# Kernel tuning notes

Measured on AMD Instinct MI355X. Metric: run time of the kernel, lower is better.

The kernel has to match this reference:

```python
import jax, jax.numpy as jnp
import numpy as np

V, D, NL, NC = 16, 256, 4, 2
MAXL, NSTATE, DCONV, EXPAND, HEADDIM = 1024, 64, 4, 2, 64
DIN = EXPAND * D            # 512 inner channels
H = DIN // HEADDIM          # 8 heads
P = HEADDIM                 # 64 head dim
CONV_DIM = DIN + 2 * NSTATE # 640 channels through depthwise conv
D_IN_PROJ = 2 * DIN + 2 * NSTATE + H  # 1160
B_, L_ = 2, 1024
EPS = 1e-5


def setup_inputs() -> dict:
    key = jax.random.key(0)
    ks = iter(jax.random.split(key, 32))

    def rn(shape, s=0.02):
        return jax.random.normal(next(ks), shape, jnp.float32) * s

    emb = rn((V, D)).at[4].set(0.0)  # padding_idx=4 row zeroed
    pos_emb = rn((MAXL, D))
    in_proj_w = rn((NL, D_IN_PROJ, D))
    conv_w = rn((NL, CONV_DIM, DCONV), 0.1)
    conv_b = rn((NL, CONV_DIM), 0.1)
    dt_bias = rn((NL, H), 0.5)
    A_log = jnp.log(jax.random.uniform(next(ks), (NL, H), jnp.float32, 1.0, 16.0))
    D_param = jnp.ones((NL, H), jnp.float32)
    norm_w = jnp.ones((NL, DIN), jnp.float32)
    out_proj_w = rn((NL, D, DIN))
    pooler_w = rn((D, D), 0.05)
    pooler_b = jnp.zeros((D,), jnp.float32)
    cls1_w = rn((D // 2, D), 0.05)
    cls1_b = jnp.zeros((D // 2,), jnp.float32)
    cls2_w = rn((NC, D // 2), 0.05)
    cls2_b = jnp.zeros((NC,), jnp.float32)
    input_ids = jax.random.randint(next(ks), (B_, L_), 0, V)
    return dict(input_ids=input_ids, emb=emb, pos_emb=pos_emb,
                in_proj_w=in_proj_w, conv_w=conv_w, conv_b=conv_b,
                dt_bias=dt_bias, A_log=A_log, D_param=D_param, norm_w=norm_w,
                out_proj_w=out_proj_w, pooler_w=pooler_w, pooler_b=pooler_b,
                cls1_w=cls1_w, cls1_b=cls1_b, cls2_w=cls2_w, cls2_b=cls2_b)


def _mamba2(x, Win, cw, cb, dtb, A_log, Dp, nw, Wout):
    Bsz, L, _ = x.shape
    zxbcdt = jnp.einsum('bld,pd->blp', x, Win)              # (B,L,2*DIN+2N+H)
    z = zxbcdt[..., :DIN]
    xBC = zxbcdt[..., DIN:DIN + CONV_DIM]
    dt = jax.nn.softplus(zxbcdt[..., -H:] + dtb)            # (B,L,H)
    # causal depthwise conv over time
    xBC = jnp.transpose(xBC, (0, 2, 1))                     # (B,C,L)
    xBC = jax.lax.conv_general_dilated(
        xBC, cw[:, None, :], (1,), [(DCONV - 1, 0)],
        dimension_numbers=('NCH', 'OIH', 'NCH'),
        feature_group_count=CONV_DIM)
    xBC = jax.nn.silu(jnp.transpose(xBC, (0, 2, 1)) + cb)   # (B,L,C)
    xs = xBC[..., :DIN].reshape(Bsz, L, H, P)
    Bm = xBC[..., DIN:DIN + NSTATE]                         # (B,L,N)
    Cm = xBC[..., DIN + NSTATE:]                            # (B,L,N)
    A = -jnp.exp(A_log)                                     # (H,)
    dA = jnp.exp(dt * A)                                    # (B,L,H)
    dBx = dt[..., None, None] * xs[..., None] * Bm[:, :, None, None, :]  # (B,L,H,P,N)

    def step(h, inp):
        dA_t, dBx_t, C_t = inp
        h = dA_t[:, :, None, None] * h + dBx_t              # (B,H,P,N)
        y = jnp.einsum('bhpn,bn->bhp', h, C_t)
        return h, y

    h0 = jnp.zeros((Bsz, H, P, NSTATE), x.dtype)
    _, y = jax.lax.scan(step, h0, (jnp.moveaxis(dA, 1, 0),
                                   jnp.moveaxis(dBx, 1, 0),
                                   jnp.moveaxis(Cm, 1, 0)))
    y = jnp.moveaxis(y, 0, 1) + Dp[None, None, :, None] * xs  # (B,L,H,P)
    y = y.reshape(Bsz, L, DIN) * jax.nn.silu(z)               # gated
    y = y * jax.lax.rsqrt(jnp.mean(y * y, axis=-1, keepdims=True) + EPS) * nw
    return jnp.einsum('bld,od->blo', y, Wout)


def reference(input_ids, emb, pos_emb, in_proj_w, conv_w, conv_b, dt_bias,
              A_log, D_param, norm_w, out_proj_w, pooler_w, pooler_b,
              cls1_w, cls1_b, cls2_w, cls2_b):
    L = input_ids.shape[1]
    x = emb[input_ids] + pos_emb[:L][None]                  # (B,L,D)
    for i in range(NL):
        x = x + _mamba2(x, in_proj_w[i], conv_w[i], conv_b[i], dt_bias[i],
                        A_log[i], D_param[i], norm_w[i], out_proj_w[i])
    pooled = (x.mean(axis=1) + x.max(axis=1)) * 0.5         # (B,D)
    pooled = jax.nn.gelu(pooled @ pooler_w.T + pooler_b, approximate=False)
    hcls = jax.nn.gelu(pooled @ cls1_w.T + cls1_b, approximate=False)
    return hcls @ cls2_w.T + cls2_b
```

## Files before the change

kernel.cpp:

```cpp
#include <hip/hip_runtime.h>
#include <math.h>

#define D_ 256
#define NL_ 4
#define NC_ 2
#define L_LEN 1024
#define NSTATE_ 64
#define DIN_ 512
#define H_ 8
#define P_ 64
#define CONVDIM_ 640
#define DPROJ_ 1160
#define EPS_ 1e-5f
#define NCH_ 16

typedef __attribute__((ext_vector_type(8))) short short8;
typedef __attribute__((ext_vector_type(4))) float f32x4;
typedef __attribute__((ext_vector_type(4))) unsigned short us4;

__device__ __forceinline__ float siluf(float x) { return x / (1.f + __expf(-x)); }
__device__ __forceinline__ float geluf(float x) { return 0.5f * x * (1.f + erff(x * 0.70710678118654752f)); }
__device__ __forceinline__ unsigned short f2bf(float f) {
    unsigned u = __float_as_uint(f);
    u += 0x7FFFu + ((u >> 16) & 1u);
    return (unsigned short)(u >> 16);
}
__device__ __forceinline__ float bf2f(unsigned short h) {
    return __uint_as_float(((unsigned)h) << 16);
}

__global__ void k_embed(const int* __restrict__ ids, const float* __restrict__ emb,
                        const float* __restrict__ pos, float* __restrict__ x, int total) {
    int i = blockIdx.x * blockDim.x + threadIdx.x;
    if (i >= total) return;
    int d = i & (D_ - 1);
    int bl = i >> 8;
    int l = bl & (L_LEN - 1);
    x[i] = emb[ids[bl] * D_ + d] + pos[l * D_ + d];
}

__global__ void k_w2bf2(const float* __restrict__ Wi, const float* __restrict__ Wo,
                        const float* __restrict__ nw,
                        unsigned short* __restrict__ wih, unsigned short* __restrict__ wil,
                        unsigned short* __restrict__ woh, unsigned short* __restrict__ wol,
                        int nin, int ntot) {
    int i = blockIdx.x * blockDim.x + threadIdx.x;
    if (i >= ntot) return;
    if (i < nin) {
        float f = Wi[i];
        unsigned short h = f2bf(f);
        wih[i] = h;
        wil[i] = f2bf(f - bf2f(h));
    } else {
        int j = i - nin;
        int layer = j / (D_ * DIN_);
        int k = j % DIN_;
        float f = Wo[j] * nw[layer * DIN_ + k];
        unsigned short h = f2bf(f);
        woh[j] = h;
        wol[j] = f2bf(f - bf2f(h));
    }
}

__global__ void __launch_bounds__(512) gemm_in(const float* __restrict__ A,
        const unsigned short* __restrict__ Bhi, const unsigned short* __restrict__ Blo,
        float* __restrict__ C, int M, int N, int K) {
    __shared__ __align__(16) unsigned short Ah[128 * 40];
    __shared__ __align__(16) unsigned short Al[128 * 40];
    __shared__ __align__(16) unsigned short Bh[64 * 40];
    __shared__ __align__(16) unsigned short Bl[64 * 40];
    const int tid = threadIdx.x;
    const int col0 = blockIdx.x * 64;
    const int row0 = blockIdx.y * 128;

    const int sar = tid >> 2, sas = (tid & 3) * 8;
    const int sbr = tid >> 2, sbs = (tid & 3) * 8;
    const bool bact = tid < 256;
    const bool bok = bact && (col0 + sbr) < N;
    const float* aptr = A + (size_t)(row0 + sar) * K + sas;
    const unsigned short* bhptr = Bhi + (size_t)(col0 + sbr) * K + sbs;
    const unsigned short* blptr = Blo + (size_t)(col0 + sbr) * K + sbs;

    float4 pa0 = *(const float4*)aptr;
    float4 pa1 = *(const float4*)(aptr + 4);
    short8 pbh = {0, 0, 0, 0, 0, 0, 0, 0}, pbl = {0, 0, 0, 0, 0, 0, 0, 0};
    if (bok) {
        pbh = *(const short8*)bhptr;
        pbl = *(const short8*)blptr;
    }

    const int wave = tid >> 6, lane = tid & 63;
    const int lq = lane >> 4, lm = lane & 15;
    f32x4 acc[4] = {};
    const int nsteps = K >> 5;
    for (int s = 0; s < nsteps; ++s) {
        __syncthreads();
        {
            float4 f = pa0;
            unsigned short h0 = f2bf(f.x), h1 = f2bf(f.y), h2 = f2bf(f.z), h3 = f2bf(f.w);
            us4 hv = {h0, h1, h2, h3};
            us4 lv = {f2bf(f.x - bf2f(h0)), f2bf(f.y - bf2f(h1)),
                      f2bf(f.z - bf2f(h2)), f2bf(f.w - bf2f(h3))};
            *(us4*)&Ah[sar * 40 + sas] = hv;
            *(us4*)&Al[sar * 40 + sas] = lv;
            f = pa1;
            h0 = f2bf(f.x); h1 = f2bf(f.y); h2 = f2bf(f.z); h3 = f2bf(f.w);
            us4 hv2 = {h0, h1, h2, h3};
            us4 lv2 = {f2bf(f.x - bf2f(h0)), f2bf(f.y - bf2f(h1)),
                       f2bf(f.z - bf2f(h2)), f2bf(f.w - bf2f(h3))};
            *(us4*)&Ah[sar * 40 + sas + 4] = hv2;
            *(us4*)&Al[sar * 40 + sas + 4] = lv2;
        }
        if (bact) {
            *(short8*)&Bh[sbr * 40 + sbs] = pbh;
            *(short8*)&Bl[sbr * 40 + sbs] = pbl;
        }
        __syncthreads();
        if (s + 1 < nsteps) {
            int ko = (s + 1) * 32;
            pa0 = *(const float4*)(aptr + ko);
            pa1 = *(const float4*)(aptr + ko + 4);
            if (bok) {
                pbh = *(const short8*)(bhptr + ko);
                pbl = *(const short8*)(blptr + ko);
            }
        }
        short8 ah = *(const short8*)&Ah[(wave * 16 + lm) * 40 + lq * 8];
        short8 al = *(const short8*)&Al[(wave * 16 + lm) * 40 + lq * 8];
#pragma unroll
        for (int ct = 0; ct < 4; ++ct) {
            short8 bh = *(const short8*)&Bh[(ct * 16 + lm) * 40 + lq * 8];
            short8 bl = *(const short8*)&Bl[(ct * 16 + lm) * 40 + lq * 8];
            acc[ct] = __builtin_amdgcn_mfma_f32_16x16x32_bf16(ah, bh, acc[ct], 0, 0, 0);
            acc[ct] = __builtin_amdgcn_mfma_f32_16x16x32_bf16(ah, bl, acc[ct], 0, 0, 0);
            acc[ct] = __builtin_amdgcn_mfma_f32_16x16x32_bf16(al, bh, acc[ct], 0, 0, 0);
        }
    }
#pragma unroll
    for (int ct = 0; ct < 4; ++ct) {
        int col = col0 + ct * 16 + lm;
        if (col >= N) continue;
        int rbase = row0 + wave * 16 + lq * 4;
#pragma unroll
        for (int reg = 0; reg < 4; ++reg) {
            C[(size_t)(rbase + reg) * N + col] = acc[ct][reg];
        }
    }
}

__global__ void __launch_bounds__(512) gemm_outs(const unsigned short* __restrict__ Ghg,
        const unsigned short* __restrict__ Glg, const float* __restrict__ rowssq,
        const unsigned short* __restrict__ Bhi, const unsigned short* __restrict__ Blo,
        float* __restrict__ x) {
    __shared__ __align__(16) unsigned short Ah[128 * 40];
    __shared__ __align__(16) unsigned short Al[128 * 40];
    __shared__ __align__(16) unsigned short Bh[64 * 40];
    __shared__ __align__(16) unsigned short Bl[64 * 40];
    const int tid = threadIdx.x;
    const int col0 = blockIdx.x * 64;
    const int row0 = blockIdx.y * 128;
    const int kbase = blockIdx.z * 128;
    const int sar = tid >> 2, sas = (tid & 3) * 8;
    const int sbr = tid >> 2, sbs = (tid & 3) * 8;
    const bool bact = tid < 256;
    const unsigned short* ahptr = Ghg + (size_t)(row0 + sar) * DIN_ + kbase + sas;
    const unsigned short* alptr = Glg + (size_t)(row0 + sar) * DIN_ + kbase + sas;
    const unsigned short* bhptr = Bhi + (size_t)(col0 + sbr) * DIN_ + kbase + sbs;
    const unsigned short* blptr = Blo + (size_t)(col0 + sbr) * DIN_ + kbase + sbs;

    short8 pah = *(const short8*)ahptr;
    short8 pal = *(const short8*)alptr;
    short8 pbh = {0, 0, 0, 0, 0, 0, 0, 0}, pbl = {0, 0, 0, 0, 0, 0, 0, 0};
    if (bact) {
        pbh = *(const short8*)bhptr;
        pbl = *(const short8*)blptr;
    }

    const int wave = tid >> 6, lane = tid & 63;
    const int lq = lane >> 4, lm = lane & 15;
    f32x4 acc[4] = {};
    for (int s = 0; s < 4; ++s) {
        __syncthreads();
        *(short8*)&Ah[sar * 40 + sas] = pah;
        *(short8*)&Al[sar * 40 + sas] = pal;
        if (bact) {
            *(short8*)&Bh[sbr * 40 + sbs] = pbh;
            *(short8*)&Bl[sbr * 40 + sbs] = pbl;
        }
        __syncthreads();
        if (s + 1 < 4) {
            int ko = (s + 1) * 32;
            pah = *(const short8*)(ahptr + ko);
            pal = *(const short8*)(alptr + ko);
            if (bact) {
                pbh = *(const short8*)(bhptr + ko);
                pbl = *(const short8*)(blptr + ko);
            }
        }
        short8 ah = *(const short8*)&Ah[(wave * 16 + lm) * 40 + lq * 8];
        short8 al = *(const short8*)&Al[(wave * 16 + lm) * 40 + lq * 8];
#pragma unroll
        for (int ct = 0; ct < 4; ++ct) {
            short8 bh = *(const short8*)&Bh[(ct * 16 + lm) * 40 + lq * 8];
            short8 bl = *(const short8*)&Bl[(ct * 16 + lm) * 40 + lq * 8];
            acc[ct] = __builtin_amdgcn_mfma_f32_16x16x32_bf16(ah, bh, acc[ct], 0, 0, 0);
            acc[ct] = __builtin_amdgcn_mfma_f32_16x16x32_bf16(ah, bl, acc[ct], 0, 0, 0);
            acc[ct] = __builtin_amdgcn_mfma_f32_16x16x32_bf16(al, bh, acc[ct], 0, 0, 0);
        }
    }
    int rbase = row0 + wave * 16 + lq * 4;
    float sc[4];
#pragma unroll
    for (int reg = 0; reg < 4; ++reg)
        sc[reg] = rsqrtf(rowssq[rbase + reg] * (1.f / DIN_) + EPS_);
#pragma unroll
    for (int ct = 0; ct < 4; ++ct) {
        int col = col0 + ct * 16 + lm;
#pragma unroll
        for (int reg = 0; reg < 4; ++reg) {
            atomicAdd(&x[(size_t)(rbase + reg) * D_ + col], sc[reg] * acc[ct][reg]);
        }
    }
}

__global__ void __launch_bounds__(512) k_ssmA(const float* __restrict__ zx,
        const float* __restrict__ cw, const float* __restrict__ cb,
        const float* __restrict__ dtbias, const float* __restrict__ Alog,
        const float* __restrict__ Dp,
        float* __restrict__ Sbuf, float* __restrict__ decay,
        float* __restrict__ Ctil, float* __restrict__ y, float* __restrict__ rowssq) {
    __shared__ float U[64][65];
    __shared__ float V[64][65];
    __shared__ float W[64][65];
    __shared__ float sdt[64], cs[64], wj[64];
    const int c = blockIdx.x, bh = blockIdx.y;
    const int b = bh >> 3, h = bh & 7;
    const int l0 = c << 6;
    const int tid = threadIdx.x, wid8 = tid >> 6, lane = tid & 63;

    if (h == 0 && tid < 64) rowssq[b * L_LEN + l0 + tid] = 0.f;

    const int chx = h * P_ + lane;
    const int chb = DIN_ + lane;
    const int chc = DIN_ + NSTATE_ + lane;
    float wx0 = cw[chx * 4], wx1 = cw[chx * 4 + 1], wx2 = cw[chx * 4 + 2], wx3 = cw[chx * 4 + 3];
    float wb0 = cw[chb * 4], wb1 = cw[chb * 4 + 1], wb2 = cw[chb * 4 + 2], wb3 = cw[chb * 4 + 3];
    float wc0 = cw[chc * 4], wc1 = cw[chc * 4 + 1], wc2 = cw[chc * 4 + 2], wc3 = cw[chc * 4 + 3];
    float bx = cb[chx], bb = cb[chb], bc = cb[chc];

    for (int r = 0; r < 64; r += 8) {
        int j = r + wid8;
        int l = l0 + j;
        float ax = bx, ab = bb, ac = bc;
#pragma unroll
        for (int k = 0; k < 4; ++k) {
            int t = l - 3 + k;
            if (t >= 0) {
                const float* row = zx + (size_t)(b * L_LEN + t) * DPROJ_;
                float wxk = (k == 0) ? wx0 : (k == 1) ? wx1 : (k == 2) ? wx2 : wx3;
                float wbk = (k == 0) ? wb0 : (k == 1) ? wb1 : (k == 2) ? wb2 : wb3;
                float wck = (k == 0) ? wc0 : (k == 1) ? wc1 : (k == 2) ? wc2 : wc3;
                ax += wxk * row[DIN_ + chx];
                ab += wbk * row[DIN_ + chb];
                ac += wck * row[DIN_ + chc];
            }
        }
        U[j][lane] = siluf(ax);
        V[j][lane] = siluf(ab);
        W[j][lane] = siluf(ac);
    }
    if (tid < 64) {
        float xv = zx[(size_t)(b * L_LEN + l0 + tid) * DPROJ_ + (DPROJ_ - H_) + h] + dtbias[h];
        float sp = fmaxf(xv, 0.f) + log1pf(__expf(-fabsf(xv)));
        sdt[tid] = sp;
        float v = sp * (-__expf(Alog[h]));
#pragma unroll
        for (int off = 1; off < 64; off <<= 1) {
            float t = __shfl_up(v, off, 64);
            if (tid >= off) v += t;
        }
        cs[tid] = v;
        float tot = __shfl(v, 63, 64);
        wj[tid] = __expf(tot - v) * sp;
        if (tid == 63) decay[bh * NCH_ + c] = __expf(tot);
    }
    __syncthreads();

    const int t4 = (tid & 15) * 4;
    const int r4 = ((tid >> 4) & 15) * 4;
    const size_t sbase = (size_t)(bh * NCH_ + c) * 4096;

    if (tid < 256) {
        float acc[4][4] = {};
        for (int j = 0; j < 64; ++j) {
            float w = wj[j];
            float4 xv = *(const float4*)&U[j][r4];
            float4 bv = *(const float4*)&V[j][t4];
            float xw[4] = {xv.x * w, xv.y * w, xv.z * w, xv.w * w};
#pragma unroll
            for (int ii = 0; ii < 4; ++ii) {
                acc[ii][0] += xw[ii] * bv.x;
                acc[ii][1] += xw[ii] * bv.y;
                acc[ii][2] += xw[ii] * bv.z;
                acc[ii][3] += xw[ii] * bv.w;
            }
        }
#pragma unroll
        for (int ii = 0; ii < 4; ++ii) {
            float4 v = {acc[ii][0], acc[ii][1], acc[ii][2], acc[ii][3]};
            *(float4*)&Sbuf[sbase + (size_t)(r4 + ii) * 64 + t4] = v;
        }
    }
    for (int r = 0; r < 64; r += 8) {
        int ii = r + wid8;
        Ctil[sbase + ii * 64 + lane] = __expf(cs[ii]) * W[ii][lane];
    }
    float wt[4][4];
    if (tid < 256) {
        float g[4][4] = {};
        for (int ng = 0; ng < 64; ng += 4) {
            float4 cf[4], bf[4];
#pragma unroll
            for (int ii = 0; ii < 4; ++ii) cf[ii] = *(const float4*)&W[r4 + ii][ng];
#pragma unroll
            for (int jj = 0; jj < 4; ++jj) bf[jj] = *(const float4*)&V[t4 + jj][ng];
#pragma unroll
            for (int ii = 0; ii < 4; ++ii)
#pragma unroll
                for (int jj = 0; jj < 4; ++jj)
                    g[ii][jj] += cf[ii].x * bf[jj].x + cf[ii].y * bf[jj].y +
                                 cf[ii].z * bf[jj].z + cf[ii].w * bf[jj].w;
        }
#pragma unroll
        for (int ii = 0; ii < 4; ++ii) {
            int i = r4 + ii;
            float csi = cs[i];
#pragma unroll
            for (int jj = 0; jj < 4; ++jj) {
                int j = t4 + jj;
                wt[ii][jj] = (j <= i) ? __expf(fminf(csi - cs[j], 0.f)) * sdt[j] * g[ii][jj] : 0.f;
            }
        }
    }
    __syncthreads();
    if (tid < 256) {
#pragma unroll
        for (int jj = 0; jj < 4; ++jj) {
            float4 v = {wt[0][jj], wt[1][jj], wt[2][jj], wt[3][jj]};
            *(float4*)&V[t4 + jj][r4] = v;
        }
    }
    __syncthreads();
    if (tid < 256) {
        float acc[4][4] = {};
        for (int j = 0; j < 64; ++j) {
            float4 wv = *(const float4*)&V[j][r4];
            float4 xv = *(const float4*)&U[j][t4];
            float ws[4] = {wv.x, wv.y, wv.z, wv.w};
#pragma unroll
            for (int ii = 0; ii < 4; ++ii) {
                acc[ii][0] += ws[ii] * xv.x;
                acc[ii][1] += ws[ii] * xv.y;
                acc[ii][2] += ws[ii] * xv.z;
                acc[ii][3] += ws[ii] * xv.w;
            }
        }
        float Dh = Dp[h];
#pragma unroll
        for (int ii = 0; ii < 4; ++ii) {
            float4 xv = *(const float4*)&U[r4 + ii][t4];
            float4 v = {acc[ii][0] + Dh * xv.x, acc[ii][1] + Dh * xv.y,
                        acc[ii][2] + Dh * xv.z, acc[ii][3] + Dh * xv.w};
            *(float4*)&y[(size_t)(b * L_LEN + l0 + r4 + ii) * DIN_ + h * P_ + t4] = v;
        }
    }
}

__global__ void __launch_bounds__(512) k_inter(const float* __restrict__ Sbuf,
        const float* __restrict__ Ctil, const float* __restrict__ decay,
        const float* __restrict__ zx, const float* __restrict__ y,
        unsigned short* __restrict__ gh, unsigned short* __restrict__ gl,
        float* __restrict__ rowssq) {
    __shared__ float Sm[64][65];
    __shared__ float Cm[64][65];
    const int c = blockIdx.x, bh = blockIdx.y;
    const int b = bh >> 3, h = bh & 7;
    const int l0 = c << 6;
    const int tid = threadIdx.x, wid8 = tid >> 6, lane = tid & 63;
    const size_t bhbase = (size_t)bh * NCH_ * 4096;

    float dec[NCH_];
#pragma unroll
    for (int k = 0; k < NCH_; ++k) dec[k] = decay[bh * NCH_ + k];

    float acc8[8] = {};
    float wgt = 1.f;
    for (int cp = c - 1; cp >= 0; --cp) {
        const float* src = Sbuf + bhbase + (size_t)cp * 4096;
#pragma unroll
        for (int i = 0; i < 8; ++i) acc8[i] += wgt * src[i * 512 + tid];
        wgt *= dec[cp];
    }
#pragma unroll
    for (int i = 0; i < 8; ++i) Sm[i * 8 + wid8][lane] = acc8[i];

    const size_t base = bhbase + (size_t)c * 4096;
    for (int r = 0; r < 64; r += 8) {
        int pp = r + wid8;
        Cm[pp][lane] = Ctil[base + pp * 64 + lane];
    }
    __syncthreads();
    const int t4 = (tid & 15) * 4;
    const int r4 = ((tid >> 4) & 15) * 4;
    if (tid < 256) {
        float acc[4][4] = {};
        if (c > 0) {
            for (int ng = 0; ng < 64; ng += 4) {
                float4 cf[4], sf[4];
#pragma unroll
                for (int ii = 0; ii < 4; ++ii) cf[ii] = *(const float4*)&Cm[r4 + ii][ng];
#pragma unroll
                for (int pp = 0; pp < 4; ++pp) sf[pp] = *(const float4*)&Sm[t4 + pp][ng];
#pragma unroll
                for (int ii = 0; ii < 4; ++ii)
#pragma unroll
                    for (int pp = 0; pp < 4; ++pp)
                        acc[ii][pp] += cf[ii].x * sf[pp].x + cf[ii].y * sf[pp].y +
                                       cf[ii].z * sf[pp].z + cf[ii].w * sf[pp].w;
            }
        }
        float ssq[4];
#pragma unroll
        for (int ii = 0; ii < 4; ++ii) {
            int row = b * L_LEN + l0 + r4 + ii;
            const float* yr = &y[(size_t)row * DIN_ + h * P_ + t4];
            const float* zr = &zx[(size_t)row * DPROJ_ + h * P_ + t4];
            float4 v = *(const float4*)yr;
            float4 z = *(const float4*)zr;
            v.x = (v.x + acc[ii][0]) * siluf(z.x);
            v.y = (v.y + acc[ii][1]) * siluf(z.y);
            v.z = (v.z + acc[ii][2]) * siluf(z.z);
            v.w = (v.w + acc[ii][3]) * siluf(z.w);
            unsigned short h0 = f2bf(v.x), h1 = f2bf(v.y), h2 = f2bf(v.z), h3 = f2bf(v.w);
            us4 hv = {h0, h1, h2, h3};
            us4 lv = {f2bf(v.x - bf2f(h0)), f2bf(v.y - bf2f(h1)),
                      f2bf(v.z - bf2f(h2)), f2bf(v.w - bf2f(h3))};
            *(us4*)&gh[(size_t)row * DIN_ + h * P_ + t4] = hv;
            *(us4*)&gl[(size_t)row * DIN_ + h * P_ + t4] = lv;
            ssq[ii] = v.x * v.x + v.y * v.y + v.z * v.z + v.w * v.w;
        }
#pragma unroll
        for (int o = 1; o < 16; o <<= 1) {
#pragma unroll
            for (int ii = 0; ii < 4; ++ii) ssq[ii] += __shfl_xor(ssq[ii], o, 64);
        }
        if ((tid & 15) == 0) {
#pragma unroll
            for (int ii = 0; ii < 4; ++ii)
                atomicAdd(&rowssq[b * L_LEN + l0 + r4 + ii], ssq[ii]);
        }
    }
}

__global__ void __launch_bounds__(1024) k_poolhead(const float* __restrict__ x,
                           const float* __restrict__ pw, const float* __restrict__ pb,
                           const float* __restrict__ c1w, const float* __restrict__ c1b,
                           const float* __restrict__ c2w, const float* __restrict__ c2b,
                           float* __restrict__ out) {
    __shared__ float ps[4][256], pm[4][256];
    __shared__ float sp[256], s1[256], s2[128];
    int b = blockIdx.x, tid = threadIdx.x;
    int t = tid & 255, grp = tid >> 8;
    const float* xb = x + (size_t)b * L_LEN * D_ + (size_t)grp * 256 * D_ + t;
    float s = 0.f, m = -INFINITY;
    for (int l = 0; l < 256; l += 4) {
        float v0 = xb[(size_t)l * D_];
        float v1 = xb[(size_t)(l + 1) * D_];
        float v2 = xb[(size_t)(l + 2) * D_];
        float v3 = xb[(size_t)(l + 3) * D_];
        s += v0 + v1 + v2 + v3;
        m = fmaxf(m, fmaxf(fmaxf(v0, v1), fmaxf(v2, v3)));
    }
    ps[grp][t] = s;
    pm[grp][t] = m;
    __syncthreads();
    if (grp == 0) {
        float ss = ps[0][t] + ps[1][t] + ps[2][t] + ps[3][t];
        float mm = fmaxf(fmaxf(pm[0][t], pm[1][t]), fmaxf(pm[2][t], pm[3][t]));
        sp[t] = (ss * (1.f / L_LEN) + mm) * 0.5f;
    }
    __syncthreads();
    if (tid < 256) {
        float acc = pb[tid];
        for (int d = 0; d < 256; ++d) acc += sp[d] * pw[tid * 256 + d];
        s1[tid] = geluf(acc);
    }
    __syncthreads();
    if (tid < 128) {
        float a = c1b[tid];
        for (int d = 0; d < 256; ++d) a += s1[d] * c1w[tid * 256 + d];
        s2[tid] = geluf(a);
    }
    __syncthreads();
    if (tid < 2) {
        float a = c2b[tid];
        for (int d = 0; d < 128; ++d) a += s2[d] * c2w[tid * 128 + d];
        out[b * NC_ + tid] = a;
    }
}

extern "C" void kernel_launch(void* const* d_in, const int* in_sizes, int n_in,
                              void* d_out, int out_size, void* d_ws, size_t ws_size,
                              hipStream_t stream) {
    const int* ids    = (const int*)d_in[0];
    const float* emb  = (const float*)d_in[1];
    const float* pos  = (const float*)d_in[2];
    const float* Wins = (const float*)d_in[3];
    const float* cw   = (const float*)d_in[4];
    const float* cb   = (const float*)d_in[5];
    const float* dtb  = (const float*)d_in[6];
    const float* Alog = (const float*)d_in[7];
    const float* Dpar = (const float*)d_in[8];
    const float* nw   = (const float*)d_in[9];
    const float* Wout = (const float*)d_in[10];
    const float* pw   = (const float*)d_in[11];
    const float* pb   = (const float*)d_in[12];
    const float* c1w  = (const float*)d_in[13];
    const float* c1b  = (const float*)d_in[14];
    const float* c2w  = (const float*)d_in[15];
    const float* c2b  = (const float*)d_in[16];
    float* out = (float*)d_out;

    const int NWIN = NL_ * DPROJ_ * D_;
    const int NWOUT = NL_ * D_ * DIN_;
    const int NG = 1048576;

    float* ws = (float*)d_ws;
    float* x      = ws;
    float* zx     = x + 524288;
    float* y      = zx + 2375680;
    float* Sbuf   = y + 1048576;
    float* Ctil   = Sbuf + 1048576;
    float* decay  = Ctil + 1048576;
    float* rowssq = decay + 256;
    unsigned short* winh = (unsigned short*)(rowssq + 2048);
    unsigned short* winl = winh + NWIN;
    unsigned short* woh  = winl + NWIN;
    unsigned short* wol  = woh + NWOUT;
    unsigned short* gh   = wol + NWOUT;
    unsigned short* gl   = gh + NG;

    k_w2bf2<<<(NWIN + NWOUT + 255) / 256, 256, 0, stream>>>(
        Wins, Wout, nw, winh, winl, woh, wol, NWIN, NWIN + NWOUT);
    k_embed<<<2048, 256, 0, stream>>>(ids, emb, pos, x, 524288);
    for (int i = 0; i < NL_; ++i) {
        size_t wo_in = (size_t)i * DPROJ_ * D_;
        size_t wo_out = (size_t)i * D_ * DIN_;
        gemm_in<<<dim3(19, 16), 512, 0, stream>>>(
            x, winh + wo_in, winl + wo_in, zx, 2048, DPROJ_, D_);
        k_ssmA<<<dim3(NCH_, 16), 512, 0, stream>>>(
            zx, cw + (size_t)i * CONVDIM_ * 4, cb + (size_t)i * CONVDIM_,
            dtb + i * H_, Alog + i * H_, Dpar + i * H_, Sbuf, decay, Ctil, y, rowssq);
        k_inter<<<dim3(NCH_, 16), 512, 0, stream>>>(Sbuf, Ctil, decay, zx, y, gh, gl, rowssq);
        gemm_outs<<<dim3(4, 16, 4), 512, 0, stream>>>(
            gh, gl, rowssq, woh + wo_out, wol + wo_out, x);
    }
    k_poolhead<<<2, 1024, 0, stream>>>(x, pw, pb, c1w, c1b, c2w, c2b, out);
}
```

Measured before the change: 373.2 us.

## Fuse SSM intra-chunk and inter-chunk kernels with flag-based cross-block sync

Merges the chunk-local SSM kernel and the inter-chunk state-passing kernel into one launch. Each block publishes its chunk state and signals through a per-chunk flag; later chunks spin-wait on earlier flags before combining states. This removes the y and Ctil round-trips through global memory and one launch per layer, and moves the rowssq zeroing into gemm_in. It relies on all 256 blocks being co-resident to avoid deadlock, and the spin-wait serialises work across chunks.

```diff
diff --git a/kernel.cpp b/kernel.cpp
--- a/kernel.cpp
+++ b/kernel.cpp
@@ -30,8 +30,10 @@
 }
 
 __global__ void k_embed(const int* __restrict__ ids, const float* __restrict__ emb,
-                        const float* __restrict__ pos, float* __restrict__ x, int total) {
+                        const float* __restrict__ pos, float* __restrict__ x,
+                        int* __restrict__ flags, int total) {
     int i = blockIdx.x * blockDim.x + threadIdx.x;
+    if (blockIdx.x == 0 && threadIdx.x < 256) flags[threadIdx.x] = 0;
     if (i >= total) return;
     int d = i & (D_ - 1);
     int bl = i >> 8;
@@ -64,12 +66,13 @@
 
 __global__ void __launch_bounds__(512) gemm_in(const float* __restrict__ A,
         const unsigned short* __restrict__ Bhi, const unsigned short* __restrict__ Blo,
-        float* __restrict__ C, int M, int N, int K) {
+        float* __restrict__ C, float* __restrict__ rowssq, int M, int N, int K) {
     __shared__ __align__(16) unsigned short Ah[128 * 40];
     __shared__ __align__(16) unsigned short Al[128 * 40];
     __shared__ __align__(16) unsigned short Bh[64 * 40];
     __shared__ __align__(16) unsigned short Bl[64 * 40];
     const int tid = threadIdx.x;
+    if (blockIdx.x == 0 && blockIdx.y < 4) rowssq[blockIdx.y * 512 + tid] = 0.f;
     const int col0 = blockIdx.x * 64;
     const int row0 = blockIdx.y * 128;
 
@@ -223,12 +226,13 @@
     }
 }
 
-__global__ void __launch_bounds__(512) k_ssmA(const float* __restrict__ zx,
+__global__ void __launch_bounds__(512) k_ssmfull(const float* __restrict__ zx,
         const float* __restrict__ cw, const float* __restrict__ cb,
         const float* __restrict__ dtbias, const float* __restrict__ Alog,
         const float* __restrict__ Dp,
         float* __restrict__ Sbuf, float* __restrict__ decay,
-        float* __restrict__ Ctil, float* __restrict__ y, float* __restrict__ rowssq) {
+        unsigned short* __restrict__ gh, unsigned short* __restrict__ gl,
+        float* __restrict__ rowssq, int* __restrict__ flags, int layerp1) {
     __shared__ float U[64][65];
     __shared__ float V[64][65];
     __shared__ float W[64][65];
@@ -238,8 +242,6 @@
     const int l0 = c << 6;
     const int tid = threadIdx.x, wid8 = tid >> 6, lane = tid & 63;
 
-    if (h == 0 && tid < 64) rowssq[b * L_LEN + l0 + tid] = 0.f;
-
     const int chx = h * P_ + lane;
     const int chb = DIN_ + lane;
     const int chc = DIN_ + NSTATE_ + lane;
@@ -247,7 +249,6 @@
     float wb0 = cw[chb * 4], wb1 = cw[chb * 4 + 1], wb2 = cw[chb * 4 + 2], wb3 = cw[chb * 4 + 3];
     float wc0 = cw[chc * 4], wc1 = cw[chc * 4 + 1], wc2 = cw[chc * 4 + 2], wc3 = cw[chc * 4 + 3];
     float bx = cb[chx], bb = cb[chb], bc = cb[chc];
-
     for (int r = 0; r < 64; r += 8) {
         int j = r + wid8;
         int l = l0 + j;
@@ -288,7 +289,8 @@
 
     const int t4 = (tid & 15) * 4;
     const int r4 = ((tid >> 4) & 15) * 4;
-    const size_t sbase = (size_t)(bh * NCH_ + c) * 4096;
+    const size_t bhbase = (size_t)bh * NCH_ * 4096;
+    const size_t sbase = bhbase + (size_t)c * 4096;
 
     if (tid < 256) {
         float acc[4][4] = {};
@@ -311,10 +313,11 @@
             *(float4*)&Sbuf[sbase + (size_t)(r4 + ii) * 64 + t4] = v;
         }
     }
-    for (int r = 0; r < 64; r += 8) {
-        int ii = r + wid8;
-        Ctil[sbase + ii * 64 + lane] = __expf(cs[ii]) * W[ii][lane];
-    }
+    __syncthreads();
+    __threadfence();
+    if (tid == 0) atomicExch(&flags[bh * NCH_ + c], layerp1);
+
+    float yacc[4][4] = {};
     float wt[4][4];
     if (tid < 256) {
         float g[4][4] = {};
@@ -352,102 +355,92 @@
     }
     __syncthreads();
     if (tid < 256) {
-        float acc[4][4] = {};
         for (int j = 0; j < 64; ++j) {
             float4 wv = *(const float4*)&V[j][r4];
             float4 xv = *(const float4*)&U[j][t4];
             float ws[4] = {wv.x, wv.y, wv.z, wv.w};
 #pragma unroll
             for (int ii = 0; ii < 4; ++ii) {
-                acc[ii][0] += ws[ii] * xv.x;
-                acc[ii][1] += ws[ii] * xv.y;
-                acc[ii][2] += ws[ii] * xv.z;
-                acc[ii][3] += ws[ii] * xv.w;
+                yacc[ii][0] += ws[ii] * xv.x;
+                yacc[ii][1] += ws[ii] * xv.y;
+                yacc[ii][2] += ws[ii] * xv.z;
+                yacc[ii][3] += ws[ii] * xv.w;
             }
         }
         float Dh = Dp[h];
 #pragma unroll
         for (int ii = 0; ii < 4; ++ii) {
             float4 xv = *(const float4*)&U[r4 + ii][t4];
-            float4 v = {acc[ii][0] + Dh * xv.x, acc[ii][1] + Dh * xv.y,
-                        acc[ii][2] + Dh * xv.z, acc[ii][3] + Dh * xv.w};
-            *(float4*)&y[(size_t)(b * L_LEN + l0 + r4 + ii) * DIN_ + h * P_ + t4] = v;
-        }
-    }
-}
-
-__global__ void __launch_bounds__(512) k_inter(const float* __restrict__ Sbuf,
-        const float* __restrict__ Ctil, const float* __restrict__ decay,
-        const float* __restrict__ zx, const float* __restrict__ y,
-        unsigned short* __restrict__ gh, unsigned short* __restrict__ gl,
-        float* __restrict__ rowssq) {
-    __shared__ float Sm[64][65];
-    __shared__ float Cm[64][65];
-    const int c = blockIdx.x, bh = blockIdx.y;
-    const int b = bh >> 3, h = bh & 7;
-    const int l0 = c << 6;
-    const int tid = threadIdx.x, wid8 = tid >> 6, lane = tid & 63;
-    const size_t bhbase = (size_t)bh * NCH_ * 4096;
-
-    float dec[NCH_];
-#pragma unroll
-    for (int k = 0; k < NCH_; ++k) dec[k] = decay[bh * NCH_ + k];
-
-    float acc8[8] = {};
-    float wgt = 1.f;
-    for (int cp = c - 1; cp >= 0; --cp) {
-        const float* src = Sbuf + bhbase + (size_t)cp * 4096;
-#pragma unroll
-        for (int i = 0; i < 8; ++i) acc8[i] += wgt * src[i * 512 + tid];
-        wgt *= dec[cp];
-    }
-#pragma unroll
-    for (int i = 0; i < 8; ++i) Sm[i * 8 + wid8][lane] = acc8[i];
-
-    const size_t base = bhbase + (size_t)c * 4096;
-    for (int r = 0; r < 64; r += 8) {
-        int pp = r + wid8;
-        Cm[pp][lane] = Ctil[base + pp * 64 + lane];
-    }
-    __syncthreads();
-    const int t4 = (tid & 15) * 4;
-    const int r4 = ((tid >> 4) & 15) * 4;
+            yacc[ii][0] += Dh * xv.x;
+            yacc[ii][1] += Dh * xv.y;
+            yacc[ii][2] += Dh * xv.z;
+            yacc[ii][3] += Dh * xv.w;
+        }
+    }
+    __syncthreads();
+
+    if (c > 0) {
+        if (tid == 0) {
+            for (int cp = 0; cp < c; ++cp) {
+                while (atomicAdd(&flags[bh * NCH_ + cp], 0) < layerp1)
+                    __builtin_amdgcn_s_sleep(8);
+            }
+        }
+        __syncthreads();
+        __threadfence();
+        float acc8[8] = {};
+        float wgt = 1.f;
+        for (int cp = c - 1; cp >= 0; --cp) {
+            const float* src = Sbuf + bhbase + (size_t)cp * 4096;
+#pragma unroll
+            for (int i = 0; i < 8; ++i) acc8[i] += wgt * src[i * 512 + tid];
+            wgt *= decay[bh * NCH_ + cp];
+        }
+#pragma unroll
+        for (int i = 0; i < 8; ++i) V[i * 8 + wid8][lane] = acc8[i];
+    }
+    __syncthreads();
+
     if (tid < 256) {
-        float acc[4][4] = {};
         if (c > 0) {
+            float acc2[4][4] = {};
             for (int ng = 0; ng < 64; ng += 4) {
                 float4 cf[4], sf[4];
 #pragma unroll
-                for (int ii = 0; ii < 4; ++ii) cf[ii] = *(const float4*)&Cm[r4 + ii][ng];
-#pragma unroll
-                for (int pp = 0; pp < 4; ++pp) sf[pp] = *(const float4*)&Sm[t4 + pp][ng];
+                for (int ii = 0; ii < 4; ++ii) cf[ii] = *(const float4*)&W[r4 + ii][ng];
+#pragma unroll
+                for (int pp = 0; pp < 4; ++pp) sf[pp] = *(const float4*)&V[t4 + pp][ng];
 #pragma unroll
                 for (int ii = 0; ii < 4; ++ii)
 #pragma unroll
                     for (int pp = 0; pp < 4; ++pp)
-                        acc[ii][pp] += cf[ii].x * sf[pp].x + cf[ii].y * sf[pp].y +
-                                       cf[ii].z * sf[pp].z + cf[ii].w * sf[pp].w;
+                        acc2[ii][pp] += cf[ii].x * sf[pp].x + cf[ii].y * sf[pp].y +
+                                        cf[ii].z * sf[pp].z + cf[ii].w * sf[pp].w;
+            }
+#pragma unroll
+            for (int ii = 0; ii < 4; ++ii) {
+                float ei = __expf(cs[r4 + ii]);
+#pragma unroll
+                for (int pp = 0; pp < 4; ++pp) yacc[ii][pp] += ei * acc2[ii][pp];
             }
         }
         float ssq[4];
 #pragma unroll
         for (int ii = 0; ii < 4; ++ii) {
             int row = b * L_LEN + l0 + r4 + ii;
-            const float* yr = &y[(size_t)row * DIN_ + h * P_ + t4];
             const float* zr = &zx[(size_t)row * DPROJ_ + h * P_ + t4];
-            float4 v = *(const float4*)yr;
             float4 z = *(const float4*)zr;
-            v.x = (v.x + acc[ii][0]) * siluf(z.x);
-            v.y = (v.y + acc[ii][1]) * siluf(z.y);
-            v.z = (v.z + acc[ii][2]) * siluf(z.z);
-            v.w = (v.w + acc[ii][3]) * siluf(z.w);
-            unsigned short h0 = f2bf(v.x), h1 = f2bf(v.y), h2 = f2bf(v.z), h3 = f2bf(v.w);
+            float v0 = yacc[ii][0] * siluf(z.x);
+            float v1 = yacc[ii][1] * siluf(z.y);
+            float v2 = yacc[ii][2] * siluf(z.z);
+            float v3 = yacc[ii][3] * siluf(z.w);
+            unsigned short h0 = f2bf(v0), h1 = f2bf(v1), h2 = f2bf(v2), h3 = f2bf(v3);
             us4 hv = {h0, h1, h2, h3};
-            us4 lv = {f2bf(v.x - bf2f(h0)), f2bf(v.y - bf2f(h1)),
-                      f2bf(v.z - bf2f(h2)), f2bf(v.w - bf2f(h3))};
+            us4 lv = {f2bf(v0 - bf2f(h0)), f2bf(v1 - bf2f(h1)),
+                      f2bf(v2 - bf2f(h2)), f2bf(v3 - bf2f(h3))};
             *(us4*)&gh[(size_t)row * DIN_ + h * P_ + t4] = hv;
             *(us4*)&gl[(size_t)row * DIN_ + h * P_ + t4] = lv;
-            ssq[ii] = v.x * v.x + v.y * v.y + v.z * v.z + v.w * v.w;
+            ssq[ii] = v0 * v0 + v1 * v1 + v2 * v2 + v3 * v3;
         }
 #pragma unroll
         for (int o = 1; o < 16; o <<= 1) {
@@ -538,12 +531,11 @@
     float* ws = (float*)d_ws;
     float* x      = ws;
     float* zx     = x + 524288;
-    float* y      = zx + 2375680;
-    float* Sbuf   = y + 1048576;
-    float* Ctil   = Sbuf + 1048576;
-    float* decay  = Ctil + 1048576;
+    float* Sbuf   = zx + 2375680;
+    float* decay  = Sbuf + 1048576;
     float* rowssq = decay + 256;
-    unsigned short* winh = (unsigned short*)(rowssq + 2048);
+    int*   flags  = (int*)(rowssq + 2048);
+    unsigned short* winh = (unsigned short*)(flags + 256);
     unsigned short* winl = winh + NWIN;
     unsigned short* woh  = winl + NWIN;
     unsigned short* wol  = woh + NWOUT;
@@ -552,16 +544,16 @@
 
     k_w2bf2<<<(NWIN + NWOUT + 255) / 256, 256, 0, stream>>>(
         Wins, Wout, nw, winh, winl, woh, wol, NWIN, NWIN + NWOUT);
-    k_embed<<<2048, 256, 0, stream>>>(ids, emb, pos, x, 524288);
+    k_embed<<<2048, 256, 0, stream>>>(ids, emb, pos, x, flags, 524288);
     for (int i = 0; i < NL_; ++i) {
         size_t wo_in = (size_t)i * DPROJ_ * D_;
         size_t wo_out = (size_t)i * D_ * DIN_;
         gemm_in<<<dim3(19, 16), 512, 0, stream>>>(
-            x, winh + wo_in, winl + wo_in, zx, 2048, DPROJ_, D_);
-        k_ssmA<<<dim3(NCH_, 16), 512, 0, stream>>>(
+            x, winh + wo_in, winl + wo_in, zx, rowssq, 2048, DPROJ_, D_);
+        k_ssmfull<<<dim3(NCH_, 16), 512, 0, stream>>>(
             zx, cw + (size_t)i * CONVDIM_ * 4, cb + (size_t)i * CONVDIM_,
-            dtb + i * H_, Alog + i * H_, Dpar + i * H_, Sbuf, decay, Ctil, y, rowssq);
-        k_inter<<<dim3(NCH_, 16), 512, 0, stream>>>(Sbuf, Ctil, decay, zx, y, gh, gl, rowssq);
+            dtb + i * H_, Alog + i * H_, Dpar + i * H_, Sbuf, decay,
+            gh, gl, rowssq, flags, i + 1);
         gemm_outs<<<dim3(4, 16, 4), 512, 0, stream>>>(
             gh, gl, rowssq, woh + wo_out, wol + wo_out, x);
     }
```

New measurement: 609.7 us. 63.3% more time.
